# Optimization experiments

Hardware: AMD Instinct MI355X
Metric: run time of the kernel (lower is better)

The kernel has to match this reference:

```python
import jax, jax.numpy as jnp
import numpy as np

B, T_OUT, T_IN = 64, 2000, 400
BLANK_LOGPROB = -1.0
NEG = -1e30  # finite stand-in for -inf (safe gradients)


def setup_inputs() -> dict:
    key = jax.random.key(0)
    k1, k2, k3 = jax.random.split(key, 3)
    attn_logprob = jax.random.normal(k1, (B, 1, T_OUT, T_IN), dtype=jnp.float32)
    in_lens = jax.random.randint(k2, (B,), T_IN // 2, T_IN + 1, dtype=jnp.int32)
    out_lens = jax.random.randint(k3, (B,), T_OUT // 2, T_OUT + 1, dtype=jnp.int32)
    return {"attn_logprob": attn_logprob, "in_lens": in_lens, "out_lens": out_lens}


def _forward_sum(attn_logprob, in_lens, out_lens):
    Bn, _, T, K = attn_logprob.shape  # (B, 1, max_query, max_key)
    dt = attn_logprob.dtype
    # pad blank class at index 0 along key dim -> (B, T, K+1)
    blank = jnp.full((Bn, 1, T, 1), BLANK_LOGPROB, dtype=dt)
    logits = jnp.concatenate([blank, attn_logprob], axis=-1)[:, 0]
    # torch code slices classes to [: key_len+1] BEFORE log_softmax -> mask then softmax
    cls = jnp.arange(K + 1)
    valid = cls[None, :] <= in_lens[:, None]  # (B, K+1)
    logits = jnp.where(valid[:, None, :], logits, NEG)
    logp = jax.nn.log_softmax(logits, axis=-1)
    logp = jnp.where(valid[:, None, :], logp, NEG)

    # CTC with target = [1..K_b]: extended states blank,1,blank,2,...,blank,K,blank
    S = 2 * K + 1
    s = jnp.arange(S)
    tok = jnp.where(s % 2 == 1, (s + 1) // 2, 0)  # class emitted in state s
    em = jnp.take(logp, tok, axis=2)              # (B, T, S)
    em_t = jnp.transpose(em, (1, 0, 2))           # (T, B, S)
    # skip transition s-2 -> s allowed for token states (all labels distinct)
    skip_ok = (s % 2 == 1) & (s >= 3)

    alpha0 = jnp.full((Bn, S), NEG, dtype=dt)
    alpha0 = alpha0.at[:, 0].set(em_t[0, :, 0]).at[:, 1].set(em_t[0, :, 1])

    def step(alpha, xt):
        em_cur, t = xt
        a1 = jnp.concatenate([jnp.full((Bn, 1), NEG, dt), alpha[:, :-1]], axis=1)
        a2 = jnp.concatenate([jnp.full((Bn, 2), NEG, dt), alpha[:, :-2]], axis=1)
        a2 = jnp.where(skip_ok[None, :], a2, NEG)
        new = em_cur + jnp.logaddexp(jnp.logaddexp(alpha, a1), a2)
        new = jnp.where((t < out_lens)[:, None], new, alpha)  # freeze past query_len
        return new, None

    ts = jnp.arange(1, T)
    alpha, _ = jax.lax.scan(step, alpha0, (em_t[1:], ts))

    last = 2 * in_lens  # final blank state index per sample
    aS = jnp.take_along_axis(alpha, last[:, None], axis=1)[:, 0]
    aSm1 = jnp.take_along_axis(alpha, (last - 1)[:, None], axis=1)[:, 0]
    ll = jnp.logaddexp(aS, aSm1)
    # nn.CTCLoss default 'mean': divide by target length; zero_infinity=True
    loss = -ll / in_lens.astype(dt)
    loss = jnp.where(jnp.isfinite(loss) & (ll > NEG / 2), loss, 0.0)
    return jnp.mean(loss)


def reference(attn_logprob, in_lens, out_lens):
    return _forward_sum(attn_logprob, in_lens, out_lens)
```

## Files before the change

kernel.cpp:

```cpp
#include <hip/hip_runtime.h>
#include <math.h>

#define TQ 2000
#define TK 400
#define NB 64
#define NW 8
#define EFF 51
#define HR 13
#define PF 26
#define NLSE 192
#define WPB 24
#define RPW 84

__device__ __forceinline__ float ex2(float x) { return __builtin_amdgcn_exp2f(x); }
__device__ __forceinline__ float lg2(float x) { return __builtin_amdgcn_logf(x); }

#define L2E 1.4426950408889634f
#define LN2f 0.6931471805599453f
#define EB 0.36787944117144233f

__device__ __forceinline__ float dpp_shr1_wave(float v, float fill) {
  return __int_as_float(__builtin_amdgcn_update_dpp(
      __float_as_int(fill), __float_as_int(v), 0x138 , 0xF, 0xF,
      false));
}
template <int CTRL, int RM>
__device__ __forceinline__ float dpp_mv(float v) {
  return __int_as_float(__builtin_amdgcn_update_dpp(
      0, __float_as_int(v), CTRL, RM, 0xF, true));
}
__device__ __forceinline__ float wave_sum_dpp(float s) {
  s = s + dpp_mv<0x111, 0xF>(s);
  s = s + dpp_mv<0x112, 0xF>(s);
  s = s + dpp_mv<0x114, 0xF>(s);
  s = s + dpp_mv<0x118, 0xF>(s);
  s = s + dpp_mv<0x142, 0xA>(s);
  s = s + dpp_mv<0x143, 0xC>(s);
  return s;
}
__device__ __forceinline__ float wave_max_dpp(float s) {
  s = fmaxf(s, dpp_mv<0x111, 0xF>(s));
  s = fmaxf(s, dpp_mv<0x112, 0xF>(s));
  s = fmaxf(s, dpp_mv<0x114, 0xF>(s));
  s = fmaxf(s, dpp_mv<0x118, 0xF>(s));
  s = fmaxf(s, dpp_mv<0x142, 0xA>(s));
  s = fmaxf(s, dpp_mv<0x143, 0xC>(s));
  return s;
}

typedef unsigned long long u64;
union F2U {
  float2 f;
  u64 u;
};

__global__ __launch_bounds__(512) void fusedA_kernel(
    const float* __restrict__ attn, const int* __restrict__ in_lens,
    const int* __restrict__ out_lens, float* __restrict__ Cpart,
    float* __restrict__ Sres) {
  const int bid = blockIdx.x;
  const int tid = threadIdx.x;
  const int w = tid >> 6, l = tid & 63;

  if (bid >= NB) {
    const int W = (bid - NB) * 8 + w;
    const int b = W / WPB;
    const int chunk = W - b * WPB;
    const int in_len = in_lens[b];
    const int out_len = out_lens[b];
    const int start = chunk * RPW;
    const int endr = min(min(start + RPW, TQ), out_len);
    const float4* base = (const float4*)(attn + (size_t)b * TQ * TK);
    const bool has2 = (l + 64) < 100;
    const int c1i = l, c2i = has2 ? (l + 64) : 35;
    const int b1 = l * 4, b2 = (l + 64) * 4;
    float acc = 0.0f;
    const int live = endr - start;
    float4 c1, c2;
    if (live > 0) {
      const float4* rp = base + (size_t)start * 100;
      c1 = rp[c1i];
      c2 = rp[c2i];
    }
    for (int i = 0; i < live; ++i) {
      float4 n1, n2;
      if (i + 1 < live) {
        const float4* rp = base + (size_t)(start + i + 1) * 100;
        n1 = rp[c1i];
        n2 = rp[c2i];
      }
      float e1a[4] = {c1.x, c1.y, c1.z, c1.w};
      float e2a[4] = {c2.x, c2.y, c2.z, c2.w};
      float s = 0.0f;
#pragma unroll
      for (int e = 0; e < 4; ++e) {
        s += (b1 + e < in_len) ? ex2(e1a[e] * L2E) : 0.0f;
        s += (has2 && (b2 + e < in_len)) ? ex2(e2a[e] * L2E) : 0.0f;
      }
      s = wave_sum_dpp(s);
      acc += lg2(s + EB);
      c1 = n1;
      c2 = n2;
    }
    if (l == 63) Cpart[b * WPB + chunk] = acc * LN2f;
    return;
  }

  const int b = bid;
  const int p = w * EFF + l;
  const int in_len = in_lens[b];
  const int out_len = out_lens[b];
  const float* __restrict__ arow = attn + (size_t)b * TQ * TK;

  const bool tokv = p < in_len;
  const int pc = (p < TK) ? p : (TK - 1);

  __shared__ float2 H[2][NW][HR];
  __shared__ __align__(16) float Wmx[2][NW];
  __shared__ float Af0[TK + 1], Af1[TK];

  float a0 = 0.0f, a1 = 0.0f;
  {
    const float x00 = arow[pc];
    if (p == 0) { a0 = EB; a1 = ex2(x00 * L2E); }
  }
  float lsum = 0.0f;

  float xq[PF];
#pragma unroll
  for (int j = 0; j < PF; ++j) {
    xq[j] = arow[(size_t)(1 + j) * TK + pc];
  }

#define STEP(SLOT, TCUR, PRED)                                      \
  {                                                                 \
    const float x = xq[SLOT];                                       \
    const int rown = ((TCUR) + PF < TQ) ? ((TCUR) + PF) : (TQ - 1); \
    xq[SLOT] = arow[(size_t)rown * TK + pc];                        \
    const float exv = tokv ? ex2(x * L2E) : 0.0f;                   \
    const float left = dpp_shr1_wave(a1, 0.0f);                     \
    const float t2 = a0 + left;                                     \
    const float n0 = t2 * EB;                                       \
    const float n1 = (t2 + a1) * exv;                               \
    if (PRED) {                                                     \
      const bool lv = (TCUR) < out_len;                             \
      a0 = lv ? n0 : a0;                                            \
      a1 = lv ? n1 : a1;                                            \
    } else {                                                        \
      a0 = n0;                                                      \
      a1 = n1;                                                      \
    }                                                               \
  }

  int hb = 0;
  for (int tb = 1; tb < out_len; tb += PF) {
#pragma unroll
    for (int h = 0; h < 2; ++h) {
      const bool fast = (tb + h * HR + HR) <= out_len;
      if (fast) {
#pragma unroll
        for (int j = 0; j < HR; ++j) STEP(h * HR + j, tb + h * HR + j, 0)
      } else {
#pragma unroll
        for (int j = 0; j < HR; ++j) STEP(h * HR + j, tb + h * HR + j, 1)
      }
      const float wm = wave_max_dpp(fmaxf(a0, a1));
      if (l >= 64 - HR) {
        F2U pv;
        pv.f = make_float2(a0, a1);
        *(volatile u64*)&H[hb][w][l - (64 - HR)] = pv.u;
      }
      if (l == 63) *(volatile float*)&Wmx[hb][w] = wm;
      asm volatile("s_waitcnt lgkmcnt(0)\ns_barrier");
      const int wsrc = (w > 0) ? (w - 1) : 0;
      const int lidx = (l < HR) ? l : 0;
      F2U hv;
      hv.u = *(volatile u64*)&H[hb][wsrc][lidx];
      const u64 m01 = *(volatile u64*)&Wmx[hb][0];
      const u64 m23 = *(volatile u64*)&Wmx[hb][2];
      const u64 m45 = *(volatile u64*)&Wmx[hb][4];
      const u64 m67 = *(volatile u64*)&Wmx[hb][6];
      if (w > 0 && l < HR) {
        a0 = hv.f.x;
        a1 = hv.f.y;
      }
      F2U c0, c1, c2, c3;
      c0.u = m01; c1.u = m23; c2.u = m45; c3.u = m67;
      const float bm = fmaxf(fmaxf(fmaxf(c0.f.x, c0.f.y), fmaxf(c1.f.x, c1.f.y)),
                             fmaxf(fmaxf(c2.f.x, c2.f.y), fmaxf(c3.f.x, c3.f.y)));
      const int e = (__float_as_int(bm) >> 23) & 0xff;
      const float sc = __int_as_float((254 - e) << 23);
      a0 *= sc;
      a1 *= sc;
      lsum += (float)(e - 127);
      hb ^= 1;
    }
  }
#undef STEP

  if ((w == 0 || l >= HR) && p <= TK) {
    Af0[p] = a0;
    if (p < TK) Af1[p] = a1;
  }
  __syncthreads();
  if (tid == 0) {
    const float ssum = Af0[in_len] + Af1[in_len - 1];
    Sres[2 * b] = ssum;
    Sres[2 * b + 1] = lsum;
  }
}

__global__ __launch_bounds__(64) void finalize_kernel(
    const float* __restrict__ Cpart, const float* __restrict__ Sres,
    const int* __restrict__ in_lens, float* __restrict__ out) {
  const int b = threadIdx.x;
  float C = 0.0f;
#pragma unroll
  for (int c = 0; c < WPB; ++c) C += Cpart[b * WPB + c];
  const float ssum = Sres[2 * b];
  const float L = Sres[2 * b + 1];
  float lb = 0.0f;
  if (ssum > 0.0f) {
    const float ll = (lg2(ssum) + L) * LN2f - C;
    lb = -ll / (float)in_lens[b];
    if (!(fabsf(lb) < 1.0e37f)) lb = 0.0f;
  }
  float v = wave_sum_dpp(lb);
  if (b == 63) out[0] = v * (1.0f / (float)NB);
}

extern "C" void kernel_launch(void* const* d_in, const int* in_sizes, int n_in,
                              void* d_out, int out_size, void* d_ws, size_t ws_size,
                              hipStream_t stream) {
  const float* attn = (const float*)d_in[0];
  const int* in_lens = (const int*)d_in[1];
  const int* out_lens = (const int*)d_in[2];
  float* Cpart = (float*)d_ws;
  float* Sres = Cpart + NB * WPB;
  float* out = (float*)d_out;

  hipLaunchKernelGGL(fusedA_kernel, dim3(NB + NLSE), dim3(512), 0, stream,
                     attn, in_lens, out_lens, Cpart, Sres);
  hipLaunchKernelGGL(finalize_kernel, dim3(1), dim3(64), 0, stream,
                     Cpart, Sres, in_lens, out);
}
```

Before: 382.1 us.

## Use four waves with two positions per lane and per-wave rescaling

The CTC alpha recursion now runs on 4 waves instead of 8. Each lane holds two adjacent key positions as packed float2 values and loads them with 8-byte loads. Each wave keeps its own log-scale exponent and rescales independently with readlane, so the block-wide max exchange is dropped. Halo exchange and barriers now happen once per 26 steps instead of every 13. In exchange each wave does more serial work, and scale reconciliation between neighbouring waves is added; the finalize kernel combines the two end states with separate exponents.

```diff
diff --git a/kernel.cpp b/kernel.cpp
--- a/kernel.cpp
+++ b/kernel.cpp
@@ -4,20 +4,30 @@
 #define TQ 2000
 #define TK 400
 #define NB 64
-#define NW 8
-#define EFF 51
-#define HR 13
+
+#define WSC 4
+#define EP 102
+#define HHALF 13
+#define GS 26
 #define PF 26
+
 #define NLSE 192
 #define WPB 24
 #define RPW 84
 
+typedef unsigned long long u64;
+typedef float f32x2 __attribute__((ext_vector_type(2)));
+
 __device__ __forceinline__ float ex2(float x) { return __builtin_amdgcn_exp2f(x); }
 __device__ __forceinline__ float lg2(float x) { return __builtin_amdgcn_logf(x); }
 
 #define L2E 1.4426950408889634f
 #define LN2f 0.6931471805599453f
 #define EB 0.36787944117144233f
+
+__device__ __forceinline__ f32x2 mk2(float a, float b) {
+  f32x2 r; r.x = a; r.y = b; return r;
+}
 
 __device__ __forceinline__ float dpp_shr1_wave(float v, float fill) {
   return __int_as_float(__builtin_amdgcn_update_dpp(
@@ -48,9 +58,8 @@
   return s;
 }
 
-typedef unsigned long long u64;
 union F2U {
-  float2 f;
+  f32x2 f;
   u64 u;
 };
 
@@ -107,106 +116,159 @@
   }
 
   const int b = bid;
-  const int p = w * EFF + l;
   const int in_len = in_lens[b];
   const int out_len = out_lens[b];
+  const int ngroups = (out_len - 2) / GS + 1;
+
+  __shared__ u64 H[2][WSC][HHALF][2];
+  __shared__ __align__(8) float Wls[2][WSC];
+  __shared__ float Af0[WSC * EP + 8];
+  __shared__ float Af1[WSC * EP + 8];
+  __shared__ float LsF[WSC];
+
+  if (w >= WSC) {
+    for (int g = 0; g < ngroups; ++g) __builtin_amdgcn_s_barrier();
+    __syncthreads();
+    return;
+  }
+
   const float* __restrict__ arow = attn + (size_t)b * TQ * TK;
-
-  const bool tokv = p < in_len;
-  const int pc = (p < TK) ? p : (TK - 1);
-
-  __shared__ float2 H[2][NW][HR];
-  __shared__ __align__(16) float Wmx[2][NW];
-  __shared__ float Af0[TK + 1], Af1[TK];
-
-  float a0 = 0.0f, a1 = 0.0f;
+  const int p0 = EP * w - GS + 2 * l;
+  const int p1 = p0 + 1;
+  const int cL = min(max(p0, 0), TK - 2);
+  const f32x2 c_msk = mk2((p0 >= 0 && p0 < in_len) ? 1.0f : 0.0f,
+                          (p1 >= 0 && p1 < in_len) ? 1.0f : 0.0f);
+
+  f32x2 A0 = mk2(0.0f, 0.0f);
+  f32x2 A1 = mk2(0.0f, 0.0f);
   {
-    const float x00 = arow[pc];
-    if (p == 0) { a0 = EB; a1 = ex2(x00 * L2E); }
+    const float x00 = arow[cL];
+    if (p0 == 0) {
+      A0.x = EB;
+      A1.x = ex2(x00 * L2E);
+    }
   }
   float lsum = 0.0f;
-
-  float xq[PF];
-#pragma unroll
-  for (int j = 0; j < PF; ++j) {
-    xq[j] = arow[(size_t)(1 + j) * TK + pc];
-  }
-
-#define STEP(SLOT, TCUR, PRED)                                      \
-  {                                                                 \
-    const float x = xq[SLOT];                                       \
-    const int rown = ((TCUR) + PF < TQ) ? ((TCUR) + PF) : (TQ - 1); \
-    xq[SLOT] = arow[(size_t)rown * TK + pc];                        \
-    const float exv = tokv ? ex2(x * L2E) : 0.0f;                   \
-    const float left = dpp_shr1_wave(a1, 0.0f);                     \
-    const float t2 = a0 + left;                                     \
-    const float n0 = t2 * EB;                                       \
-    const float n1 = (t2 + a1) * exv;                               \
-    if (PRED) {                                                     \
-      const bool lv = (TCUR) < out_len;                             \
-      a0 = lv ? n0 : a0;                                            \
-      a1 = lv ? n1 : a1;                                            \
-    } else {                                                        \
-      a0 = n0;                                                      \
-      a1 = n1;                                                      \
-    }                                                               \
+  bool mzero = true;
+
+  f32x2 xq[PF];
+#pragma unroll
+  for (int j = 0; j < PF; ++j)
+    xq[j] = *(const f32x2*)(arow + (size_t)(1 + j) * TK + cL);
+
+#define STEP(SLOT, TCUR, PRED)                                        \
+  {                                                                   \
+    const f32x2 x = xq[SLOT];                                         \
+    const int rown = ((TCUR) + PF < TQ) ? ((TCUR) + PF) : (TQ - 1);   \
+    xq[SLOT] = *(const f32x2*)(arow + (size_t)rown * TK + cL);        \
+    const f32x2 ev = mk2(ex2(x.x * L2E), ex2(x.y * L2E)) * c_msk;     \
+    const float left = dpp_shr1_wave(A1.y, 0.0f);                     \
+    const f32x2 t2 = A0 + mk2(left, A1.x);                            \
+    const f32x2 n1 = (t2 + A1) * ev;                                  \
+    const f32x2 n0 = t2 * EB;                                         \
+    if (PRED) {                                                       \
+      if ((TCUR) < out_len) {            \
+        A0 = n0;                                                      \
+        A1 = n1;                                                      \
+      }                                                               \
+    } else {                                                          \
+      A0 = n0;                                                        \
+      A1 = n1;                                                        \
+    }                                                                 \
+  }
+
+#define RESCALE()                                                     \
+  {                                                                   \
+    float m4 = fmaxf(fmaxf(A0.x, A0.y), fmaxf(A1.x, A1.y));           \
+    float wmx = wave_max_dpp(m4);                                     \
+    const float bm = __int_as_float(                                  \
+        __builtin_amdgcn_readlane(__float_as_int(wmx), 63));          \
+    if (bm > 0.0f) {                                                  \
+      const int e = (__float_as_int(bm) >> 23) & 0xff;                \
+      const float sc = __int_as_float((254 - e) << 23);               \
+      A0 = A0 * sc;                                                   \
+      A1 = A1 * sc;                                                   \
+      lsum += (float)(e - 127);                                       \
+      mzero = false;                                                  \
+    } else {                                                          \
+      mzero = true;                                                   \
+    }                                                                 \
   }
 
   int hb = 0;
-  for (int tb = 1; tb < out_len; tb += PF) {
+  for (int tb = 1; tb < out_len; tb += GS) {
 #pragma unroll
     for (int h = 0; h < 2; ++h) {
-      const bool fast = (tb + h * HR + HR) <= out_len;
+      const bool fast = (tb + h * HHALF + HHALF) <= out_len;
       if (fast) {
 #pragma unroll
-        for (int j = 0; j < HR; ++j) STEP(h * HR + j, tb + h * HR + j, 0)
+        for (int j = 0; j < HHALF; ++j)
+          STEP(h * HHALF + j, tb + h * HHALF + j, 0)
       } else {
 #pragma unroll
-        for (int j = 0; j < HR; ++j) STEP(h * HR + j, tb + h * HR + j, 1)
-      }
-      const float wm = wave_max_dpp(fmaxf(a0, a1));
-      if (l >= 64 - HR) {
-        F2U pv;
-        pv.f = make_float2(a0, a1);
-        *(volatile u64*)&H[hb][w][l - (64 - HR)] = pv.u;
-      }
-      if (l == 63) *(volatile float*)&Wmx[hb][w] = wm;
-      asm volatile("s_waitcnt lgkmcnt(0)\ns_barrier");
-      const int wsrc = (w > 0) ? (w - 1) : 0;
-      const int lidx = (l < HR) ? l : 0;
-      F2U hv;
-      hv.u = *(volatile u64*)&H[hb][wsrc][lidx];
-      const u64 m01 = *(volatile u64*)&Wmx[hb][0];
-      const u64 m23 = *(volatile u64*)&Wmx[hb][2];
-      const u64 m45 = *(volatile u64*)&Wmx[hb][4];
-      const u64 m67 = *(volatile u64*)&Wmx[hb][6];
-      if (w > 0 && l < HR) {
-        a0 = hv.f.x;
-        a1 = hv.f.y;
-      }
-      F2U c0, c1, c2, c3;
-      c0.u = m01; c1.u = m23; c2.u = m45; c3.u = m67;
-      const float bm = fmaxf(fmaxf(fmaxf(c0.f.x, c0.f.y), fmaxf(c1.f.x, c1.f.y)),
-                             fmaxf(fmaxf(c2.f.x, c2.f.y), fmaxf(c3.f.x, c3.f.y)));
-      const int e = (__float_as_int(bm) >> 23) & 0xff;
-      const float sc = __int_as_float((254 - e) << 23);
-      a0 *= sc;
-      a1 *= sc;
-      lsum += (float)(e - 127);
-      hb ^= 1;
-    }
+        for (int j = 0; j < HHALF; ++j)
+          STEP(h * HHALF + j, tb + h * HHALF + j, 1)
+      }
+      RESCALE()
+    }
+    if (l >= 64 - HHALF) {
+      F2U h0, h1;
+      h0.f = mk2(A0.x, A1.x);
+      h1.f = mk2(A0.y, A1.y);
+      volatile u64* hp = (volatile u64*)&H[hb][w][l - (64 - HHALF)][0];
+      hp[0] = h0.u;
+      hp[1] = h1.u;
+    }
+    if (l == 63) *(volatile float*)&Wls[hb][w] = lsum;
+    asm volatile("s_waitcnt lgkmcnt(0)\ns_barrier");
+    const int wsrc = (w > 0) ? (w - 1) : 0;
+    const int lidx = (l < HHALF) ? l : 0;
+    F2U r0, r1;
+    volatile u64* rp = (volatile u64*)&H[hb][wsrc][lidx][0];
+    r0.u = rp[0];
+    r1.u = rp[1];
+    const float Lp = *(volatile float*)&Wls[hb][wsrc];
+    if (w > 0) {
+      const float delta = Lp - lsum;
+      float sfh;
+      if (mzero) {
+        lsum = Lp;
+        sfh = 1.0f;
+      } else if (delta > 0.0f) {
+        const float so = ex2(-delta);
+        A0 = A0 * so;
+        A1 = A1 * so;
+        lsum = Lp;
+        sfh = 1.0f;
+      } else {
+        sfh = ex2(delta);
+      }
+      if (l < HHALF) {
+        A0.x = r0.f.x * sfh;
+        A1.x = r0.f.y * sfh;
+        A0.y = r1.f.x * sfh;
+        A1.y = r1.f.y * sfh;
+      }
+      RESCALE()
+    }
+    hb ^= 1;
   }
 #undef STEP
-
-  if ((w == 0 || l >= HR) && p <= TK) {
-    Af0[p] = a0;
-    if (p < TK) Af1[p] = a1;
-  }
+#undef RESCALE
+
+  if (l >= HHALF) {
+    Af0[p0] = A0.x;
+    Af1[p0] = A1.x;
+    Af0[p1] = A0.y;
+    Af1[p1] = A1.y;
+  }
+  if (l == 0) LsF[w] = lsum;
   __syncthreads();
   if (tid == 0) {
-    const float ssum = Af0[in_len] + Af1[in_len - 1];
-    Sres[2 * b] = ssum;
-    Sres[2 * b + 1] = lsum;
+    Sres[4 * b + 0] = Af0[in_len];
+    Sres[4 * b + 1] = LsF[in_len / EP];
+    Sres[4 * b + 2] = Af1[in_len - 1];
+    Sres[4 * b + 3] = LsF[(in_len - 1) / EP];
   }
 }
 
@@ -217,11 +279,17 @@
   float C = 0.0f;
 #pragma unroll
   for (int c = 0; c < WPB; ++c) C += Cpart[b * WPB + c];
-  const float ssum = Sres[2 * b];
-  const float L = Sres[2 * b + 1];
+  const float v0 = Sres[4 * b + 0];
+  const float e0 = Sres[4 * b + 1];
+  const float v1 = Sres[4 * b + 2];
+  const float e1 = Sres[4 * b + 3];
   float lb = 0.0f;
-  if (ssum > 0.0f) {
-    const float ll = (lg2(ssum) + L) * LN2f - C;
+  if (v0 > 0.0f || v1 > 0.0f) {
+    const float l0 = (v0 > 0.0f) ? (lg2(v0) + e0) : -3.0e38f;
+    const float l1 = (v1 > 0.0f) ? (lg2(v1) + e1) : -3.0e38f;
+    const float mm = fmaxf(l0, l1);
+    const float ll2 = mm + lg2(ex2(l0 - mm) + ex2(l1 - mm));
+    const float ll = ll2 * LN2f - C;
     lb = -ll / (float)in_lens[b];
     if (!(fabsf(lb) < 1.0e37f)) lb = 0.0f;
   }
```

Measured after the change: 378.6 us. Within noise of the previous version (-0.9%).
